# Kernel tuning notes

Hardware: AMD Instinct MI355X
Metric: run time of the kernel (lower is better)

Reference implementation:

```python
import jax, jax.numpy as jnp
import numpy as np

N_NODES = 100000
N_EDGES = 3200000
HIDDEN = 64
NUM_LABELS = 1000
NUM_GRAPHS = 128


def setup_inputs() -> dict:
    key = jax.random.key(0)
    ks = jax.random.split(key, 12)
    node_labels = jax.random.randint(ks[0], (N_NODES,), 0, NUM_LABELS)
    edge_index = jax.random.randint(ks[1], (2, N_EDGES), 0, N_NODES)
    edge_weight = jax.random.uniform(ks[2], (N_EDGES,), dtype=jnp.float32)
    batch = jnp.sort(jax.random.randint(ks[3], (N_NODES,), 0, NUM_GRAPHS))
    s = 1.0 / np.sqrt(HIDDEN)
    emb = jax.random.normal(ks[4], (NUM_LABELS, HIDDEN), dtype=jnp.float32)
    W1 = jax.random.normal(ks[5], (HIDDEN, HIDDEN), dtype=jnp.float32) * s
    b1 = jnp.zeros((HIDDEN,), dtype=jnp.float32)
    W2 = jax.random.normal(ks[6], (HIDDEN, HIDDEN), dtype=jnp.float32) * s
    b2 = jnp.zeros((HIDDEN,), dtype=jnp.float32)
    W3 = jax.random.normal(ks[7], (HIDDEN, HIDDEN), dtype=jnp.float32) * s
    b3 = jnp.zeros((HIDDEN,), dtype=jnp.float32)
    W4 = jax.random.normal(ks[8], (HIDDEN, 1), dtype=jnp.float32) * s
    b4 = jnp.zeros((1,), dtype=jnp.float32)
    return {"node_labels": node_labels, "edge_index": edge_index,
            "edge_weight": edge_weight, "batch": batch, "emb": emb,
            "W1": W1, "b1": b1, "W2": W2, "b2": b2,
            "W3": W3, "b3": b3, "W4": W4, "b4": b4}


def _gcn_conv(x, W, b, src, dst, ew):
    # PyG GCNConv: add self-loops (weight 1), symmetric D^-1/2 normalization.
    h = x @ W                                               # [N, H]
    deg = jax.ops.segment_sum(ew, dst, num_segments=N_NODES) + 1.0  # self-loop
    dinv = jax.lax.rsqrt(deg)                               # [N]
    norm = dinv[src] * ew * dinv[dst]                       # [E]
    out = jax.ops.segment_sum(h[src] * norm[:, None], dst, num_segments=N_NODES)
    out = out + h * (dinv * dinv)[:, None]                  # self-loop message
    return out + b


def reference(node_labels, edge_index, edge_weight, batch, emb,
              W1, b1, W2, b2, W3, b3, W4, b4):
    src, dst = edge_index[0], edge_index[1]
    x = emb[node_labels]                                    # [N, H]
    x = jax.nn.relu(_gcn_conv(x, W1, b1, src, dst, edge_weight))
    x = jax.nn.relu(_gcn_conv(x, W2, b2, src, dst, edge_weight))
    # global mean pool over graphs (dropout is identity in eval mode)
    sums = jax.ops.segment_sum(x, batch, num_segments=NUM_GRAPHS)   # [G, H]
    cnts = jax.ops.segment_sum(jnp.ones((N_NODES,), x.dtype), batch,
                               num_segments=NUM_GRAPHS)
    g = sums / jnp.maximum(cnts, 1.0)[:, None]
    g = jax.nn.relu(g @ W3 + b3)
    return jnp.squeeze(g @ W4 + b4, axis=-1)                # [G]
```

## Files before the change

### kernel.cpp

```cpp
#include <hip/hip_runtime.h>
#include <hip/hip_fp16.h>

#define N_NODES    100000
#define N_EDGES    3200000
#define HIDDEN     64
#define NUM_GRAPHS 128
#define NUM_LABELS 1000

#define BKT_SHIFT  8
#define NPB        256
#define NBKT       ((N_NODES + NPB - 1) / NPB)
#define ENTCAP     8960
#define BSLOT      ENTCAP
#define SCHUNK     4096
#define SNBLK      ((N_EDGES + SCHUNK - 1) / SCHUNK)
#define CPT        ((SNBLK + 255) / 256)

__global__ __launch_bounds__(256) void hist_blk_kernel(
    const int* __restrict__ dst, int* __restrict__ cnt, int E) {
    __shared__ int h[NBKT];
    int t = threadIdx.x;
    for (int b = t; b < NBKT; b += 256) h[b] = 0;
    __syncthreads();
    int base = blockIdx.x * SCHUNK;
    int end  = min(base + SCHUNK, E);
    for (int i = base + t; i < end; i += 256)
        atomicAdd(&h[dst[i] >> BKT_SHIFT], 1);
    __syncthreads();
    int* o = cnt + (size_t)blockIdx.x * NBKT;
    for (int b = t; b < NBKT; b += 256) o[b] = h[b];
}

__global__ __launch_bounds__(256) void scan_cols_kernel(
    const int* __restrict__ cnt, int* __restrict__ basem, int* __restrict__ bktTot) {
    __shared__ int a[256], bsh[256];
    int b = blockIdx.x;
    int t = threadIdx.x;
    int v[CPT];
    int loc = 0;
    int blk0 = t * CPT;
    #pragma unroll
    for (int j = 0; j < CPT; ++j) {
        int blk = blk0 + j;
        int c = (blk < SNBLK) ? cnt[(size_t)blk * NBKT + b] : 0;
        v[j] = loc;
        loc += c;
    }
    a[t] = loc; __syncthreads();
    int* pa = a; int* pb = bsh;
    #pragma unroll
    for (int d = 1; d < 256; d <<= 1) {
        int x = pa[t];
        if (t >= d) x += pa[t - d];
        pb[t] = x; __syncthreads();
        int* tmp = pa; pa = pb; pb = tmp;
    }
    int ex = (t == 0) ? 0 : pa[t - 1];
    #pragma unroll
    for (int j = 0; j < CPT; ++j) {
        int blk = blk0 + j;
        if (blk < SNBLK) basem[(size_t)blk * NBKT + b] = ex + v[j];
    }
    if (t == 255) bktTot[b] = pa[255];
}

__global__ __launch_bounds__(512) void scan_buckets_kernel(const int* __restrict__ bktTot,
                                                           int* __restrict__ boff) {
    __shared__ int a[512], b[512];
    int t = threadIdx.x;
    int v = (t < NBKT) ? bktTot[t] : 0;
    a[t] = v; __syncthreads();
    int* pa = a; int* pb = b;
    #pragma unroll
    for (int d = 1; d < 512; d <<= 1) {
        int x = pa[t];
        if (t >= d) x += pa[t - d];
        pb[t] = x; __syncthreads();
        int* tmp = pa; pa = pb; pb = tmp;
    }
    int ex = (t == 0) ? 0 : pa[t - 1];
    if (t < NBKT) boff[t] = ex;
    if (t == NBKT - 1) boff[NBKT] = pa[t];
}

__global__ __launch_bounds__(256) void scatter_kernel(
    const int* __restrict__ src, const int* __restrict__ dst,
    const float* __restrict__ ew, const int* __restrict__ cnt,
    const int* __restrict__ basem, int2* __restrict__ barr, int E) {
    __shared__ int2 ent[SCHUNK];
    __shared__ int  gaddr[SCHUNK];
    __shared__ int  h[NBKT];
    __shared__ int  ls[NBKT];
    __shared__ int  a[256], bsc[256];
    int t = threadIdx.x;
    int blk = blockIdx.x;
    const int* cn = cnt   + (size_t)blk * NBKT;
    const int* bm = basem + (size_t)blk * NBKT;
    int i0 = 2 * t, i1 = 2 * t + 1;
    int c0 = (i0 < NBKT) ? cn[i0] : 0;
    int c1 = (i1 < NBKT) ? cn[i1] : 0;
    a[t] = c0 + c1; __syncthreads();
    int* pa = a; int* pb = bsc;
    #pragma unroll
    for (int d = 1; d < 256; d <<= 1) {
        int x = pa[t];
        if (t >= d) x += pa[t - d];
        pb[t] = x; __syncthreads();
        int* tmp = pa; pa = pb; pb = tmp;
    }
    int ex = (t == 0) ? 0 : pa[t - 1];
    if (i0 < NBKT) { ls[i0] = ex;      h[i0] = 0; }
    if (i1 < NBKT) { ls[i1] = ex + c0; h[i1] = 0; }
    __syncthreads();
    int base = blk * SCHUNK;
    int end  = min(base + SCHUNK, E);
    int m    = end - base;
    for (int i = base + t; i < end; i += 256) {
        int d  = dst[i];
        int bk = d >> BKT_SHIFT;
        int p  = atomicAdd(&h[bk], 1);
        int j  = ls[bk] + p;
        ent[j]   = make_int2(src[i] | ((d & (NPB - 1)) << 20), __float_as_int(ew[i]));
        gaddr[j] = bk * BSLOT + bm[bk] + p;
    }
    __syncthreads();
    for (int j = t; j < m; j += 256) barr[gaddr[j]] = ent[j];
}

__global__ __launch_bounds__(256) void dinv_bucket_kernel(
    const int2* __restrict__ barr, const int* __restrict__ bktTot,
    float* __restrict__ dinv) {
    __shared__ float wsum[NPB];
    int b = blockIdx.x, t = threadIdx.x;
    wsum[t] = 0.f;
    __syncthreads();
    int m = bktTot[b];
    const int2* bs = barr + (size_t)b * BSLOT;
    for (int i = t; i < m; i += 256) {
        int2 v = bs[i];
        atomicAdd(&wsum[(v.x >> 20) & (NPB - 1)], __int_as_float(v.y));
    }
    __syncthreads();
    int node = (b << BKT_SHIFT) + t;
    if (node < N_NODES) dinv[node] = rsqrtf(wsum[t] + 1.0f);
}

__global__ __launch_bounds__(256) void finalize_kernel(
    const int2* __restrict__ barr, const int* __restrict__ boff,
    const int* __restrict__ labels, const float* __restrict__ dinv,
    int2* __restrict__ csr, int* __restrict__ off) {
    __shared__ int2  ent[ENTCAP];
    __shared__ int   hcnt[NPB];
    __shared__ float ldv[NPB];
    __shared__ int   ha[NPB], hcur[NPB];
    int b = blockIdx.x;
    int t = threadIdx.x;
    int s = boff[b], e = boff[b + 1];
    int m = e - s;
    const int2* bsrc = barr + (size_t)b * BSLOT;
    int node0 = b << BKT_SHIFT;
    int nn = min(NPB, N_NODES - node0);
    hcnt[t] = 0;
    ldv[t]  = (t < nn) ? dinv[node0 + t] : 0.f;
    __syncthreads();
    bool staged = (m <= ENTCAP);
    for (int i = t; i < m; i += 256) {
        int2 v = bsrc[i];
        if (staged) ent[i] = v;
        atomicAdd(&hcnt[(v.x >> 20) & (NPB - 1)], 1);
    }
    __syncthreads();
    ha[t] = hcnt[t];
    __syncthreads();
    #pragma unroll
    for (int d = 1; d < NPB; d <<= 1) {
        int x = ha[t];
        if (t >= d) x += ha[t - d];
        __syncthreads();
        ha[t] = x;
        __syncthreads();
    }
    {
        int ex = (t == 0) ? 0 : ha[t - 1];
        hcur[t] = s + ex;
        if (t < nn) off[node0 + t] = s + ex;
    }
    if (b == NBKT - 1 && t == 0) off[N_NODES] = e;
    __syncthreads();
    for (int i = t; i < m; i += 256) {
        int2 v = staged ? ent[i] : bsrc[i];
        int doff = (v.x >> 20) & (NPB - 1);
        int sv   = v.x & 0xFFFFF;
        float wf = __int_as_float(v.y) * ldv[doff] * dinv[sv];
        int lab  = labels[sv];
        int p = atomicAdd(&hcur[doff], 1);
        csr[p] = make_int2(sv | (lab << 17), __float_as_int(wf));
    }
}

__global__ __launch_bounds__(256) void ew1_kernel(
    const float* __restrict__ emb, const float* __restrict__ W,
    __half* __restrict__ OUTH) {
    __shared__ float Ws[64 * 64];
    __shared__ float Xs[64 * 65];
    int t = threadIdx.x;
    #pragma unroll
    for (int s = 0; s < 16; ++s) Ws[s * 256 + t] = W[s * 256 + t];
    int r0   = blockIdx.x * 64;
    int lrow = t >> 2;
    int c0   = (t & 3) * 16;
    int grow = r0 + lrow;
    const float* srcrow = (grow < NUM_LABELS) ? (emb + (size_t)grow * HIDDEN) : emb;
    #pragma unroll
    for (int c = 0; c < 16; c += 4) {
        float4 v = *(const float4*)(srcrow + c0 + c);
        Xs[lrow * 65 + c0 + c + 0] = v.x;
        Xs[lrow * 65 + c0 + c + 1] = v.y;
        Xs[lrow * 65 + c0 + c + 2] = v.z;
        Xs[lrow * 65 + c0 + c + 3] = v.w;
    }
    __syncthreads();
    int row = t & 63;
    int j0  = (t >> 6) * 16;
    float4 a0 = make_float4(0,0,0,0), a1 = a0, a2 = a0, a3 = a0;
    #pragma unroll
    for (int k = 0; k < 64; ++k) {
        float xv = Xs[row * 65 + k];
        const float4* wr = (const float4*)(Ws + k * 64 + j0);
        float4 w0 = wr[0], w1 = wr[1], w2 = wr[2], w3 = wr[3];
        a0.x = fmaf(xv, w0.x, a0.x); a0.y = fmaf(xv, w0.y, a0.y);
        a0.z = fmaf(xv, w0.z, a0.z); a0.w = fmaf(xv, w0.w, a0.w);
        a1.x = fmaf(xv, w1.x, a1.x); a1.y = fmaf(xv, w1.y, a1.y);
        a1.z = fmaf(xv, w1.z, a1.z); a1.w = fmaf(xv, w1.w, a1.w);
        a2.x = fmaf(xv, w2.x, a2.x); a2.y = fmaf(xv, w2.y, a2.y);
        a2.z = fmaf(xv, w2.z, a2.z); a2.w = fmaf(xv, w2.w, a2.w);
        a3.x = fmaf(xv, w3.x, a3.x); a3.y = fmaf(xv, w3.y, a3.y);
        a3.z = fmaf(xv, w3.z, a3.z); a3.w = fmaf(xv, w3.w, a3.w);
    }
    int gr = r0 + row;
    if (gr < NUM_LABELS) {
        union { __half2 h2[8]; uint4 u4[2]; } pk;
        pk.h2[0] = __floats2half2_rn(a0.x, a0.y);
        pk.h2[1] = __floats2half2_rn(a0.z, a0.w);
        pk.h2[2] = __floats2half2_rn(a1.x, a1.y);
        pk.h2[3] = __floats2half2_rn(a1.z, a1.w);
        pk.h2[4] = __floats2half2_rn(a2.x, a2.y);
        pk.h2[5] = __floats2half2_rn(a2.z, a2.w);
        pk.h2[6] = __floats2half2_rn(a3.x, a3.y);
        pk.h2[7] = __floats2half2_rn(a3.z, a3.w);
        uint4* o = (uint4*)(OUTH + (size_t)gr * HIDDEN + j0);
        o[0] = pk.u4[0]; o[1] = pk.u4[1];
    }
}

#define ACC8(rv_, wv_) { \
    const __half2* hp_ = (const __half2*)&(rv_); \
    float2 f0_ = __half22float2(hp_[0]); \
    float2 f1_ = __half22float2(hp_[1]); \
    float2 f2_ = __half22float2(hp_[2]); \
    float2 f3_ = __half22float2(hp_[3]); \
    accA.x = fmaf(f0_.x, (wv_), accA.x); accA.y = fmaf(f0_.y, (wv_), accA.y); \
    accA.z = fmaf(f1_.x, (wv_), accA.z); accA.w = fmaf(f1_.y, (wv_), accA.w); \
    accB.x = fmaf(f2_.x, (wv_), accB.x); accB.y = fmaf(f2_.y, (wv_), accB.y); \
    accB.z = fmaf(f3_.x, (wv_), accB.z); accB.w = fmaf(f3_.y, (wv_), accB.w); }

#define RED8(of_) { \
    accA.x += __shfl_xor(accA.x, of_, 64); accA.y += __shfl_xor(accA.y, of_, 64); \
    accA.z += __shfl_xor(accA.z, of_, 64); accA.w += __shfl_xor(accA.w, of_, 64); \
    accB.x += __shfl_xor(accB.x, of_, 64); accB.y += __shfl_xor(accB.y, of_, 64); \
    accB.z += __shfl_xor(accB.z, of_, 64); accB.w += __shfl_xor(accB.w, of_, 64); }

__global__ __launch_bounds__(256) void agg1_kernel(
    const __half* __restrict__ EW1h, const int* __restrict__ labels,
    const int2* __restrict__ csr, const int* __restrict__ off,
    const float* __restrict__ dinv, const float* __restrict__ bias,
    __half* __restrict__ A1h, int n) {
    int wid  = (blockIdx.x * blockDim.x + threadIdx.x) >> 6;
    if (wid >= n) return;
    int lane = threadIdx.x & 63;
    int q = lane & 7, g = lane >> 3;
    int i   = off[wid] + g;
    int end = off[wid + 1];
    float4 accA = make_float4(0.f,0.f,0.f,0.f), accB = accA;
    while (i < end) {
        int2 e0 = csr[i];
        int2 e1 = (i + 8  < end) ? csr[i + 8]  : make_int2(0, 0);
        int2 e2 = (i + 16 < end) ? csr[i + 16] : make_int2(0, 0);
        int2 e3 = (i + 24 < end) ? csr[i + 24] : make_int2(0, 0);
        uint4 r0 = *(const uint4*)(EW1h + (size_t)((unsigned)e0.x >> 17) * HIDDEN + q * 8);
        uint4 r1 = *(const uint4*)(EW1h + (size_t)((unsigned)e1.x >> 17) * HIDDEN + q * 8);
        uint4 r2 = *(const uint4*)(EW1h + (size_t)((unsigned)e2.x >> 17) * HIDDEN + q * 8);
        uint4 r3 = *(const uint4*)(EW1h + (size_t)((unsigned)e3.x >> 17) * HIDDEN + q * 8);
        float w0 = __int_as_float(e0.y);
        float w1 = __int_as_float(e1.y);
        float w2 = __int_as_float(e2.y);
        float w3 = __int_as_float(e3.y);
        ACC8(r0, w0); ACC8(r1, w1); ACC8(r2, w2); ACC8(r3, w3);
        i += 32;
    }
    RED8(8); RED8(16); RED8(32);
    if (g == 0) {
        float di  = dinv[wid];
        float di2 = di * di;
        int labw = labels[wid];
        uint4 xu = *(const uint4*)(EW1h + (size_t)labw * HIDDEN + q * 8);
        const __half2* xp = (const __half2*)&xu;
        float2 x0 = __half22float2(xp[0]);
        float2 x1 = __half22float2(xp[1]);
        float2 x2 = __half22float2(xp[2]);
        float2 x3 = __half22float2(xp[3]);
        const float4* bp = (const float4*)(bias + q * 8);
        float4 bv0 = bp[0], bv1 = bp[1];
        float4 vA, vB;
        vA.x = fmaxf(fmaf(x0.x, di2, accA.x) + bv0.x, 0.f);
        vA.y = fmaxf(fmaf(x0.y, di2, accA.y) + bv0.y, 0.f);
        vA.z = fmaxf(fmaf(x1.x, di2, accA.z) + bv0.z, 0.f);
        vA.w = fmaxf(fmaf(x1.y, di2, accA.w) + bv0.w, 0.f);
        vB.x = fmaxf(fmaf(x2.x, di2, accB.x) + bv1.x, 0.f);
        vB.y = fmaxf(fmaf(x2.y, di2, accB.y) + bv1.y, 0.f);
        vB.z = fmaxf(fmaf(x3.x, di2, accB.z) + bv1.z, 0.f);
        vB.w = fmaxf(fmaf(x3.y, di2, accB.w) + bv1.w, 0.f);
        union { __half2 h2[4]; uint4 u4; } pk;
        pk.h2[0] = __floats2half2_rn(vA.x, vA.y);
        pk.h2[1] = __floats2half2_rn(vA.z, vA.w);
        pk.h2[2] = __floats2half2_rn(vB.x, vB.y);
        pk.h2[3] = __floats2half2_rn(vB.z, vB.w);
        *(uint4*)(A1h + (size_t)wid * HIDDEN + q * 8) = pk.u4;
    }
}

__global__ __launch_bounds__(256) void agg2_kernel(
    const __half* __restrict__ Xh,
    const int2* __restrict__ csr, const int* __restrict__ off,
    const float* __restrict__ dinv, float* __restrict__ OUT, int n) {
    int wid  = (blockIdx.x * blockDim.x + threadIdx.x) >> 6;
    if (wid >= n) return;
    int lane = threadIdx.x & 63;
    int q = lane & 7, g = lane >> 3;
    int i   = off[wid] + g;
    int end = off[wid + 1];
    float4 accA = make_float4(0.f,0.f,0.f,0.f), accB = accA;
    while (i < end) {
        int2 e0 = csr[i];
        int2 e1 = (i + 8  < end) ? csr[i + 8]  : make_int2(0, 0);
        int2 e2 = (i + 16 < end) ? csr[i + 16] : make_int2(0, 0);
        int2 e3 = (i + 24 < end) ? csr[i + 24] : make_int2(0, 0);
        uint4 r0 = *(const uint4*)(Xh + (size_t)(e0.x & 0x1FFFF) * HIDDEN + q * 8);
        uint4 r1 = *(const uint4*)(Xh + (size_t)(e1.x & 0x1FFFF) * HIDDEN + q * 8);
        uint4 r2 = *(const uint4*)(Xh + (size_t)(e2.x & 0x1FFFF) * HIDDEN + q * 8);
        uint4 r3 = *(const uint4*)(Xh + (size_t)(e3.x & 0x1FFFF) * HIDDEN + q * 8);
        float w0 = __int_as_float(e0.y);
        float w1 = __int_as_float(e1.y);
        float w2 = __int_as_float(e2.y);
        float w3 = __int_as_float(e3.y);
        ACC8(r0, w0); ACC8(r1, w1); ACC8(r2, w2); ACC8(r3, w3);
        i += 32;
    }
    RED8(8); RED8(16); RED8(32);
    if (g == 0) {
        float di  = dinv[wid];
        float di2 = di * di;
        uint4 xu = *(const uint4*)(Xh + (size_t)wid * HIDDEN + q * 8);
        const __half2* xp = (const __half2*)&xu;
        float2 x0 = __half22float2(xp[0]);
        float2 x1 = __half22float2(xp[1]);
        float2 x2 = __half22float2(xp[2]);
        float2 x3 = __half22float2(xp[3]);
        accA.x = fmaf(x0.x, di2, accA.x);
        accA.y = fmaf(x0.y, di2, accA.y);
        accA.z = fmaf(x1.x, di2, accA.z);
        accA.w = fmaf(x1.y, di2, accA.w);
        accB.x = fmaf(x2.x, di2, accB.x);
        accB.y = fmaf(x2.y, di2, accB.y);
        accB.z = fmaf(x3.x, di2, accB.z);
        accB.w = fmaf(x3.y, di2, accB.w);
        float* o = OUT + (size_t)wid * HIDDEN + q * 8;
        *(float4*)o       = accA;
        *(float4*)(o + 4) = accB;
    }
}

__global__ __launch_bounds__(256) void gemm2_kernel(
    const float* __restrict__ X, const float* __restrict__ W,
    const float* __restrict__ bias, float* __restrict__ OUT, int n) {
    __shared__ float Ws[64 * 64];
    __shared__ float Xs[64 * 65];
    int t = threadIdx.x;
    #pragma unroll
    for (int s = 0; s < 16; ++s) Ws[s * 256 + t] = W[s * 256 + t];
    int r0   = blockIdx.x * 64;
    int lrow = t >> 2;
    int c0   = (t & 3) * 16;
    const float* srcrow = ((r0 + lrow) < n) ? (X + (size_t)(r0 + lrow) * HIDDEN) : X;
    #pragma unroll
    for (int c = 0; c < 16; c += 4) {
        float4 v = *(const float4*)(srcrow + c0 + c);
        Xs[lrow * 65 + c0 + c + 0] = v.x;
        Xs[lrow * 65 + c0 + c + 1] = v.y;
        Xs[lrow * 65 + c0 + c + 2] = v.z;
        Xs[lrow * 65 + c0 + c + 3] = v.w;
    }
    __syncthreads();
    int row = t & 63;
    int j0  = (t >> 6) * 16;
    float4 a0 = *(const float4*)(bias + j0 + 0);
    float4 a1 = *(const float4*)(bias + j0 + 4);
    float4 a2 = *(const float4*)(bias + j0 + 8);
    float4 a3 = *(const float4*)(bias + j0 + 12);
    #pragma unroll
    for (int k = 0; k < 64; ++k) {
        float xv = Xs[row * 65 + k];
        const float4* wr = (const float4*)(Ws + k * 64 + j0);
        float4 w0 = wr[0], w1 = wr[1], w2 = wr[2], w3 = wr[3];
        a0.x = fmaf(xv, w0.x, a0.x); a0.y = fmaf(xv, w0.y, a0.y);
        a0.z = fmaf(xv, w0.z, a0.z); a0.w = fmaf(xv, w0.w, a0.w);
        a1.x = fmaf(xv, w1.x, a1.x); a1.y = fmaf(xv, w1.y, a1.y);
        a1.z = fmaf(xv, w1.z, a1.z); a1.w = fmaf(xv, w1.w, a1.w);
        a2.x = fmaf(xv, w2.x, a2.x); a2.y = fmaf(xv, w2.y, a2.y);
        a2.z = fmaf(xv, w2.z, a2.z); a2.w = fmaf(xv, w2.w, a2.w);
        a3.x = fmaf(xv, w3.x, a3.x); a3.y = fmaf(xv, w3.y, a3.y);
        a3.z = fmaf(xv, w3.z, a3.z); a3.w = fmaf(xv, w3.w, a3.w);
    }
    int gr = r0 + row;
    if (gr < n) {
        float4* o = (float4*)(OUT + (size_t)gr * HIDDEN + j0);
        a0.x = fmaxf(a0.x, 0.f); a0.y = fmaxf(a0.y, 0.f); a0.z = fmaxf(a0.z, 0.f); a0.w = fmaxf(a0.w, 0.f);
        a1.x = fmaxf(a1.x, 0.f); a1.y = fmaxf(a1.y, 0.f); a1.z = fmaxf(a1.z, 0.f); a1.w = fmaxf(a1.w, 0.f);
        a2.x = fmaxf(a2.x, 0.f); a2.y = fmaxf(a2.y, 0.f); a2.z = fmaxf(a2.z, 0.f); a2.w = fmaxf(a2.w, 0.f);
        a3.x = fmaxf(a3.x, 0.f); a3.y = fmaxf(a3.y, 0.f); a3.z = fmaxf(a3.z, 0.f); a3.w = fmaxf(a3.w, 0.f);
        o[0] = a0; o[1] = a1; o[2] = a2; o[3] = a3;
    }
}

__global__ __launch_bounds__(256) void pool_head_kernel(
    const float* __restrict__ A, const int* __restrict__ batch,
    const float* __restrict__ W3, const float* __restrict__ b3,
    const float* __restrict__ W4, const float* __restrict__ b4,
    float* __restrict__ out) {
    __shared__ int   sb[2];
    __shared__ float sd[4][64];
    __shared__ float gv[64];
    int gidx = blockIdx.x;
    int t = threadIdx.x;
    if (t < 2) {
        int target = gidx + t;
        int lo = 0, hi = N_NODES;
        while (lo < hi) {
            int mid = (lo + hi) >> 1;
            if (batch[mid] < target) lo = mid + 1; else hi = mid;
        }
        sb[t] = lo;
    }
    __syncthreads();
    int start = sb[0], end = sb[1];
    int col = t & 63, rg = t >> 6;
    float sum = 0.f;
    for (int r = start + rg; r < end; r += 4) sum += A[(size_t)r * HIDDEN + col];
    sd[rg][col] = sum;
    __syncthreads();
    if (t < 64) {
        float tot = sd[0][col] + sd[1][col] + sd[2][col] + sd[3][col];
        float cnt = (float)(end - start);
        gv[col] = tot / fmaxf(cnt, 1.0f);
    }
    __syncthreads();
    if (t < 64) {
        float acc = b3[t];
        #pragma unroll
        for (int k = 0; k < 64; ++k) acc = fmaf(gv[k], W3[k * 64 + t], acc);
        float p = fmaxf(acc, 0.f) * W4[t];
        #pragma unroll
        for (int o = 32; o > 0; o >>= 1) p += __shfl_down(p, o, 64);
        if (t == 0) out[gidx] = p + b4[0];
    }
}

extern "C" void kernel_launch(void* const* d_in, const int* in_sizes, int n_in,
                              void* d_out, int out_size, void* d_ws, size_t ws_size,
                              hipStream_t stream) {
    const int*   labels = (const int*)d_in[0];
    const int*   ei     = (const int*)d_in[1];
    const int*   src    = ei;
    const int*   dst    = ei + N_EDGES;
    const float* ew     = (const float*)d_in[2];
    const int*   batch  = (const int*)d_in[3];
    const float* emb    = (const float*)d_in[4];
    const float* W1 = (const float*)d_in[5],  *b1 = (const float*)d_in[6];
    const float* W2 = (const float*)d_in[7],  *b2 = (const float*)d_in[8];
    const float* W3 = (const float*)d_in[9],  *b3 = (const float*)d_in[10];
    const float* W4 = (const float*)d_in[11], *b4 = (const float*)d_in[12];
    float* out = (float*)d_out;

    float* ws   = (float*)d_ws;
    float* bufH = ws;
    float* bufA = bufH + (size_t)N_NODES * HIDDEN;
    int2*  csr  = (int2*)(bufA + (size_t)N_NODES * HIDDEN);
    int*   boff   = (int*)(csr + N_EDGES);
    int*   bktTot = boff + NBKT + 1;
    int*   off    = bktTot + NBKT;
    float* dinv   = (float*)(off + N_NODES + 1);
    __half* EW1h  = (__half*)(dinv + N_NODES);
    int2*  barr   = (int2*)ws;
    __half* A1h   = (__half*)bufA;
    float* A2     = bufA;
    int*   cnt    = (int*)csr;
    int*   basem  = cnt + (size_t)SNBLK * NBKT;

    const int NT = 256;
    const int blkW = (N_NODES * 64 + NT - 1) / NT;
    const int blkG = (N_NODES + 63) / 64;

    hist_blk_kernel<<<SNBLK, NT, 0, stream>>>(dst, cnt, N_EDGES);
    scan_cols_kernel<<<NBKT, NT, 0, stream>>>(cnt, basem, bktTot);
    scan_buckets_kernel<<<1, 512, 0, stream>>>(bktTot, boff);
    scatter_kernel<<<SNBLK, NT, 0, stream>>>(src, dst, ew, cnt, basem, barr, N_EDGES);
    dinv_bucket_kernel<<<NBKT, NT, 0, stream>>>(barr, bktTot, dinv);
    finalize_kernel<<<NBKT, NT, 0, stream>>>(barr, boff, labels, dinv, csr, off);

    ew1_kernel<<<(NUM_LABELS + 63) / 64, NT, 0, stream>>>(emb, W1, EW1h);
    agg1_kernel<<<blkW, NT, 0, stream>>>(EW1h, labels, csr, off, dinv, b1, A1h, N_NODES);

    agg2_kernel<<<blkW, NT, 0, stream>>>(A1h, csr, off, dinv, bufH, N_NODES);
    gemm2_kernel<<<blkG, NT, 0, stream>>>(bufH, W2, b2, A2, N_NODES);

    pool_head_kernel<<<NUM_GRAPHS, NT, 0, stream>>>(A2, batch, W3, b3, W4, b4, out);
}
```

Before: 414.2 us.

## Fuse degree computation into finalize, refactor normalization, store layer-2 output in half

Removes the separate dinv kernel by accumulating weighted degrees inside finalize_kernel, so the bucketed edge array is read once instead of twice. The source-side dinv factor is no longer baked into CSR weights: agg1 multiplies by dinv[src] per edge (an extra gather), and agg1's output is prescaled by dinv so agg2 can use plain dst-side weights. gemm2 now writes fp16 output, and pool_head uses 1024 threads to read it, halving that traffic. The risks are the extra random dinv loads in agg1 and lower precision in the pooled activations.

Measured after the change: 349.5 us (median of 2 runs). 15.6% less time.

```diff
diff --git a/kernel.cpp b/kernel.cpp
--- a/kernel.cpp
+++ b/kernel.cpp
@@ -127,30 +127,13 @@
     for (int j = t; j < m; j += 256) barr[gaddr[j]] = ent[j];
 }
 
-__global__ __launch_bounds__(256) void dinv_bucket_kernel(
-    const int2* __restrict__ barr, const int* __restrict__ bktTot,
-    float* __restrict__ dinv) {
-    __shared__ float wsum[NPB];
-    int b = blockIdx.x, t = threadIdx.x;
-    wsum[t] = 0.f;
-    __syncthreads();
-    int m = bktTot[b];
-    const int2* bs = barr + (size_t)b * BSLOT;
-    for (int i = t; i < m; i += 256) {
-        int2 v = bs[i];
-        atomicAdd(&wsum[(v.x >> 20) & (NPB - 1)], __int_as_float(v.y));
-    }
-    __syncthreads();
-    int node = (b << BKT_SHIFT) + t;
-    if (node < N_NODES) dinv[node] = rsqrtf(wsum[t] + 1.0f);
-}
-
 __global__ __launch_bounds__(256) void finalize_kernel(
     const int2* __restrict__ barr, const int* __restrict__ boff,
-    const int* __restrict__ labels, const float* __restrict__ dinv,
-    int2* __restrict__ csr, int* __restrict__ off) {
+    const int* __restrict__ labels,
+    int2* __restrict__ csr, int* __restrict__ off, float* __restrict__ dinv) {
     __shared__ int2  ent[ENTCAP];
     __shared__ int   hcnt[NPB];
+    __shared__ float wsum[NPB];
     __shared__ float ldv[NPB];
     __shared__ int   ha[NPB], hcur[NPB];
     int b = blockIdx.x;
@@ -160,14 +143,15 @@
     const int2* bsrc = barr + (size_t)b * BSLOT;
     int node0 = b << BKT_SHIFT;
     int nn = min(NPB, N_NODES - node0);
-    hcnt[t] = 0;
-    ldv[t]  = (t < nn) ? dinv[node0 + t] : 0.f;
+    hcnt[t] = 0; wsum[t] = 0.f;
     __syncthreads();
     bool staged = (m <= ENTCAP);
     for (int i = t; i < m; i += 256) {
         int2 v = bsrc[i];
         if (staged) ent[i] = v;
-        atomicAdd(&hcnt[(v.x >> 20) & (NPB - 1)], 1);
+        int doff = (v.x >> 20) & (NPB - 1);
+        atomicAdd(&hcnt[doff], 1);
+        atomicAdd(&wsum[doff], __int_as_float(v.y));
     }
     __syncthreads();
     ha[t] = hcnt[t];
@@ -183,7 +167,12 @@
     {
         int ex = (t == 0) ? 0 : ha[t - 1];
         hcur[t] = s + ex;
-        if (t < nn) off[node0 + t] = s + ex;
+        float dv = rsqrtf(wsum[t] + 1.0f);
+        ldv[t] = dv;
+        if (t < nn) {
+            off[node0 + t]  = s + ex;
+            dinv[node0 + t] = dv;
+        }
     }
     if (b == NBKT - 1 && t == 0) off[N_NODES] = e;
     __syncthreads();
@@ -191,7 +180,7 @@
         int2 v = staged ? ent[i] : bsrc[i];
         int doff = (v.x >> 20) & (NPB - 1);
         int sv   = v.x & 0xFFFFF;
-        float wf = __int_as_float(v.y) * ldv[doff] * dinv[sv];
+        float wf = __int_as_float(v.y) * ldv[doff];
         int lab  = labels[sv];
         int p = atomicAdd(&hcur[doff], 1);
         csr[p] = make_int2(sv | (lab << 17), __float_as_int(wf));
@@ -291,10 +280,10 @@
         uint4 r1 = *(const uint4*)(EW1h + (size_t)((unsigned)e1.x >> 17) * HIDDEN + q * 8);
         uint4 r2 = *(const uint4*)(EW1h + (size_t)((unsigned)e2.x >> 17) * HIDDEN + q * 8);
         uint4 r3 = *(const uint4*)(EW1h + (size_t)((unsigned)e3.x >> 17) * HIDDEN + q * 8);
-        float w0 = __int_as_float(e0.y);
-        float w1 = __int_as_float(e1.y);
-        float w2 = __int_as_float(e2.y);
-        float w3 = __int_as_float(e3.y);
+        float w0 = __int_as_float(e0.y) * dinv[e0.x & 0x1FFFF];
+        float w1 = __int_as_float(e1.y) * dinv[e1.x & 0x1FFFF];
+        float w2 = __int_as_float(e2.y) * dinv[e2.x & 0x1FFFF];
+        float w3 = __int_as_float(e3.y) * dinv[e3.x & 0x1FFFF];
         ACC8(r0, w0); ACC8(r1, w1); ACC8(r2, w2); ACC8(r3, w3);
         i += 32;
     }
@@ -321,10 +310,10 @@
         vB.z = fmaxf(fmaf(x3.x, di2, accB.z) + bv1.z, 0.f);
         vB.w = fmaxf(fmaf(x3.y, di2, accB.w) + bv1.w, 0.f);
         union { __half2 h2[4]; uint4 u4; } pk;
-        pk.h2[0] = __floats2half2_rn(vA.x, vA.y);
-        pk.h2[1] = __floats2half2_rn(vA.z, vA.w);
-        pk.h2[2] = __floats2half2_rn(vB.x, vB.y);
-        pk.h2[3] = __floats2half2_rn(vB.z, vB.w);
+        pk.h2[0] = __floats2half2_rn(di * vA.x, di * vA.y);
+        pk.h2[1] = __floats2half2_rn(di * vA.z, di * vA.w);
+        pk.h2[2] = __floats2half2_rn(di * vB.x, di * vB.y);
+        pk.h2[3] = __floats2half2_rn(di * vB.z, di * vB.w);
         *(uint4*)(A1h + (size_t)wid * HIDDEN + q * 8) = pk.u4;
     }
 }
@@ -359,21 +348,20 @@
     RED8(8); RED8(16); RED8(32);
     if (g == 0) {
         float di  = dinv[wid];
-        float di2 = di * di;
         uint4 xu = *(const uint4*)(Xh + (size_t)wid * HIDDEN + q * 8);
         const __half2* xp = (const __half2*)&xu;
         float2 x0 = __half22float2(xp[0]);
         float2 x1 = __half22float2(xp[1]);
         float2 x2 = __half22float2(xp[2]);
         float2 x3 = __half22float2(xp[3]);
-        accA.x = fmaf(x0.x, di2, accA.x);
-        accA.y = fmaf(x0.y, di2, accA.y);
-        accA.z = fmaf(x1.x, di2, accA.z);
-        accA.w = fmaf(x1.y, di2, accA.w);
-        accB.x = fmaf(x2.x, di2, accB.x);
-        accB.y = fmaf(x2.y, di2, accB.y);
-        accB.z = fmaf(x3.x, di2, accB.z);
-        accB.w = fmaf(x3.y, di2, accB.w);
+        accA.x = fmaf(x0.x, di, accA.x);
+        accA.y = fmaf(x0.y, di, accA.y);
+        accA.z = fmaf(x1.x, di, accA.z);
+        accA.w = fmaf(x1.y, di, accA.w);
+        accB.x = fmaf(x2.x, di, accB.x);
+        accB.y = fmaf(x2.y, di, accB.y);
+        accB.z = fmaf(x3.x, di, accB.z);
+        accB.w = fmaf(x3.y, di, accB.w);
         float* o = OUT + (size_t)wid * HIDDEN + q * 8;
         *(float4*)o       = accA;
         *(float4*)(o + 4) = accB;
@@ -382,7 +370,7 @@
 
 __global__ __launch_bounds__(256) void gemm2_kernel(
     const float* __restrict__ X, const float* __restrict__ W,
-    const float* __restrict__ bias, float* __restrict__ OUT, int n) {
+    const float* __restrict__ bias, __half* __restrict__ OUT, int n) {
     __shared__ float Ws[64 * 64];
     __shared__ float Xs[64 * 65];
     int t = threadIdx.x;
@@ -423,22 +411,31 @@
     }
     int gr = r0 + row;
     if (gr < n) {
-        float4* o = (float4*)(OUT + (size_t)gr * HIDDEN + j0);
         a0.x = fmaxf(a0.x, 0.f); a0.y = fmaxf(a0.y, 0.f); a0.z = fmaxf(a0.z, 0.f); a0.w = fmaxf(a0.w, 0.f);
         a1.x = fmaxf(a1.x, 0.f); a1.y = fmaxf(a1.y, 0.f); a1.z = fmaxf(a1.z, 0.f); a1.w = fmaxf(a1.w, 0.f);
         a2.x = fmaxf(a2.x, 0.f); a2.y = fmaxf(a2.y, 0.f); a2.z = fmaxf(a2.z, 0.f); a2.w = fmaxf(a2.w, 0.f);
         a3.x = fmaxf(a3.x, 0.f); a3.y = fmaxf(a3.y, 0.f); a3.z = fmaxf(a3.z, 0.f); a3.w = fmaxf(a3.w, 0.f);
-        o[0] = a0; o[1] = a1; o[2] = a2; o[3] = a3;
-    }
-}
-
-__global__ __launch_bounds__(256) void pool_head_kernel(
-    const float* __restrict__ A, const int* __restrict__ batch,
+        union { __half2 h2[8]; uint4 u4[2]; } pk;
+        pk.h2[0] = __floats2half2_rn(a0.x, a0.y);
+        pk.h2[1] = __floats2half2_rn(a0.z, a0.w);
+        pk.h2[2] = __floats2half2_rn(a1.x, a1.y);
+        pk.h2[3] = __floats2half2_rn(a1.z, a1.w);
+        pk.h2[4] = __floats2half2_rn(a2.x, a2.y);
+        pk.h2[5] = __floats2half2_rn(a2.z, a2.w);
+        pk.h2[6] = __floats2half2_rn(a3.x, a3.y);
+        pk.h2[7] = __floats2half2_rn(a3.z, a3.w);
+        uint4* o = (uint4*)(OUT + (size_t)gr * HIDDEN + j0);
+        o[0] = pk.u4[0]; o[1] = pk.u4[1];
+    }
+}
+
+__global__ __launch_bounds__(1024) void pool_head_kernel(
+    const __half* __restrict__ A, const int* __restrict__ batch,
     const float* __restrict__ W3, const float* __restrict__ b3,
     const float* __restrict__ W4, const float* __restrict__ b4,
     float* __restrict__ out) {
     __shared__ int   sb[2];
-    __shared__ float sd[4][64];
+    __shared__ float sd[16][64];
     __shared__ float gv[64];
     int gidx = blockIdx.x;
     int t = threadIdx.x;
@@ -455,11 +452,14 @@
     int start = sb[0], end = sb[1];
     int col = t & 63, rg = t >> 6;
     float sum = 0.f;
-    for (int r = start + rg; r < end; r += 4) sum += A[(size_t)r * HIDDEN + col];
+    for (int r = start + rg; r < end; r += 16)
+        sum += __half2float(A[(size_t)r * HIDDEN + col]);
     sd[rg][col] = sum;
     __syncthreads();
     if (t < 64) {
-        float tot = sd[0][col] + sd[1][col] + sd[2][col] + sd[3][col];
+        float tot = 0.f;
+        #pragma unroll
+        for (int j = 0; j < 16; ++j) tot += sd[j][col];
         float cnt = (float)(end - start);
         gv[col] = tot / fmaxf(cnt, 1.0f);
     }
@@ -502,7 +502,7 @@
     __half* EW1h  = (__half*)(dinv + N_NODES);
     int2*  barr   = (int2*)ws;
     __half* A1h   = (__half*)bufA;
-    float* A2     = bufA;
+    __half* A2h   = (__half*)bufA;
     int*   cnt    = (int*)csr;
     int*   basem  = cnt + (size_t)SNBLK * NBKT;
 
@@ -514,14 +514,13 @@
     scan_cols_kernel<<<NBKT, NT, 0, stream>>>(cnt, basem, bktTot);
     scan_buckets_kernel<<<1, 512, 0, stream>>>(bktTot, boff);
     scatter_kernel<<<SNBLK, NT, 0, stream>>>(src, dst, ew, cnt, basem, barr, N_EDGES);
-    dinv_bucket_kernel<<<NBKT, NT, 0, stream>>>(barr, bktTot, dinv);
-    finalize_kernel<<<NBKT, NT, 0, stream>>>(barr, boff, labels, dinv, csr, off);
+    finalize_kernel<<<NBKT, NT, 0, stream>>>(barr, boff, labels, csr, off, dinv);
 
     ew1_kernel<<<(NUM_LABELS + 63) / 64, NT, 0, stream>>>(emb, W1, EW1h);
     agg1_kernel<<<blkW, NT, 0, stream>>>(EW1h, labels, csr, off, dinv, b1, A1h, N_NODES);
 
     agg2_kernel<<<blkW, NT, 0, stream>>>(A1h, csr, off, dinv, bufH, N_NODES);
-    gemm2_kernel<<<blkG, NT, 0, stream>>>(bufH, W2, b2, A2, N_NODES);
-
-    pool_head_kernel<<<NUM_GRAPHS, NT, 0, stream>>>(A2, batch, W3, b3, W4, b4, out);
-}
+    gemm2_kernel<<<blkG, NT, 0, stream>>>(bufH, W2, b2, A2h, N_NODES);
+
+    pool_head_kernel<<<NUM_GRAPHS, 1024, 0, stream>>>(A2h, batch, W3, b3, W4, b4, out);
+}
```
